# Performance work log

Measured on AMD Instinct MI355X. Metric: run time of the kernel, lower is better.

The kernel has to match this reference:

```python
import jax, jax.numpy as jnp
import numpy as np

B, S, D, H, HD = 8, 1024, 1152, 16, 72
L, R = 32, 36  # get_decompose_dim(1152)
W_BITS, A_BITS = 4, 8


def _ste_round(x):
    return x + jax.lax.stop_gradient(jnp.round(x) - x)


def _fake_quant(x, bits):
    # symmetric fake quant, per last-dim group (per-token for acts, per-out-channel for weights)
    qmax = 2.0 ** (bits - 1) - 1.0
    scale = jnp.maximum(jnp.max(jnp.abs(x), axis=-1, keepdims=True) / qmax, 1e-8)
    return jnp.clip(_ste_round(x / scale), -qmax - 1.0, qmax) * scale


def _kron_apply(x, A, Bm):
    # DecomposeTransMatrix: x (..., L*R) -> reshape (L,R), Y = A^T X B (row-vector kron transform)
    sh = x.shape
    y = jnp.einsum('...lr,lp,rq->...pq', x.reshape(sh[:-1] + (L, R)), A, Bm)
    return y.reshape(sh)


def setup_inputs() -> dict:
    key = jax.random.key(0)
    ks = jax.random.split(key, 16)
    lin = lambda k, sh: jax.random.normal(k, sh, jnp.float32) * 0.02
    return {
        'hidden_states': jax.random.normal(ks[0], (B, S, D), jnp.float32),
        'Wq': lin(ks[1], (D, D)), 'bq': lin(ks[2], (D,)),
        'Wk': lin(ks[3], (D, D)), 'bk': lin(ks[4], (D,)),
        'Wv': lin(ks[5], (D, D)), 'bv': lin(ks[6], (D,)),
        'Wo': lin(ks[7], (D, D)), 'bo': lin(ks[8], (D,)),
        'ln_A': jnp.eye(L, dtype=jnp.float32) + 0.02 * jax.random.normal(ks[9], (L, L), jnp.float32),
        'ln_B': jnp.eye(R, dtype=jnp.float32) + 0.02 * jax.random.normal(ks[10], (R, R), jnp.float32),
        'ln_diag': 1.0 + 0.1 * jax.random.uniform(ks[11], (D,), jnp.float32),
        'vc': jnp.eye(HD, dtype=jnp.float32) + 0.02 * jax.random.normal(ks[12], (HD, HD), jnp.float32),
        'o_mat': jnp.eye(H, dtype=jnp.float32) + 0.02 * jax.random.normal(ks[13], (H, H), jnp.float32),
    }


def reference(hidden_states, Wq, bq, Wk, bk, Wv, bv, Wo, bo, ln_A, ln_B, ln_diag, vc, o_mat):
    invA_T = jnp.linalg.inv(ln_A).T
    invB_T = jnp.linalg.inv(ln_B).T
    # ln_trans applied to activations (diag scale + decomposed Kronecker rotation)
    x = _kron_apply(hidden_states * ln_diag, ln_A, ln_B)  # (B,S,D)

    def qlinear(xin, W, b, out_vc=None):
        # qa_trans inv_t folded into weight: W' = kron(W/diag, invA.T, invB.T) over input dim
        Wt = _kron_apply(W * (1.0 / ln_diag), invA_T, invB_T)
        bt = b
        if out_vc is not None:  # vc_trans folded into to_v output channels
            Wt = jnp.einsum('hdi,de->hei', Wt.reshape(H, HD, D), out_vc).reshape(D, D)
            bt = (b.reshape(H, HD) @ out_vc).reshape(-1)
        return _fake_quant(xin, A_BITS) @ _fake_quant(Wt, W_BITS).T + bt

    q = qlinear(x, Wq, bq).reshape(B, S, H, HD).transpose(0, 2, 1, 3)  # (B,H,S,HD)
    k = qlinear(x, Wk, bk).reshape(B, S, H, HD).transpose(0, 2, 1, 3)
    v = qlinear(x, Wv, bv, out_vc=vc).reshape(B, S, H, HD).transpose(0, 2, 1, 3)

    # baddbmm with beta=0, alpha=1: NO 1/sqrt(d) scaling (faithful to source)
    scores = jnp.einsum('bhqd,bhkd->bhqk', q, k)
    attn = jax.nn.softmax(scores.astype(jnp.float32), axis=-1).astype(q.dtype)
    ctx = jnp.einsum('bhqk,bhkd->bhqd', attn, v).transpose(0, 2, 1, 3)  # (B,S,H,HD)

    # o_trans: matmul(o_mat.T, Y) per token
    ctx = jnp.einsum('bsgd,gh->bshd', ctx, o_mat).reshape(B, S, D)

    # to_out with qa_trans=[inv(O).T, inv(V).T] folded into weight
    o_it = jnp.linalg.inv(o_mat).T
    v_it = jnp.linalg.inv(vc).T
    Wot = jnp.einsum('gh,ogd,de->ohe', o_it, Wo.reshape(D, H, HD), v_it).reshape(D, D)
    out = _fake_quant(ctx, A_BITS) @ _fake_quant(Wot, W_BITS).T + bo
    return out  # rescale_output_factor = 1.0
```

## Files before the change

kernel.cpp:

```cpp
#include <hip/hip_runtime.h>
#include <hip/hip_bf16.h>

#define BB 8
#define SS 1024
#define DD 1152
#define HH 16
#define HD 72
#define PD 96
#define LL 32
#define RR 36
#define NTOK (BB*SS)

typedef __attribute__((ext_vector_type(8)))  short short8;
typedef __attribute__((ext_vector_type(4)))  float f32x4;
typedef __attribute__((ext_vector_type(16))) float f32x16;
typedef __attribute__((ext_vector_type(4)))  unsigned short ushort4v;

#define F_IAT   0
#define F_IBT   1024
#define F_IO    2320
#define F_IV    2576
#define F_BVT   7760
#define F_SX    16384
#define F_SWQ   24576
#define F_SWK   25728
#define F_SWV   26880
#define F_SWO   28032
#define F_SCTX  32768
#define B_R1    1048576ULL
#define B_WB    (B_R1 + 37748736ULL)
#define B_XB    (B_WB + 4ULL*2654208ULL)
#define B_QB    (B_XB + 18874368ULL)
#define B_KB    (B_QB + 25165824ULL)
#define B_VB    (B_KB + 25165824ULL)
#define B_VT    (B_VB + 25165824ULL)
#define WSLOT   1327104ULL

__device__ __forceinline__ unsigned bf16rne(float f) {
    unsigned u = __builtin_bit_cast(unsigned, f);
    return (u + 0x7fffu + ((u >> 16) & 1u)) >> 16;
}
__device__ __forceinline__ unsigned cvtpk(float lo, float hi) {
    unsigned r;
    asm("v_cvt_pk_bf16_f32 %0, %1, %2" : "=v"(r) : "v"(lo), "v"(hi));
    return r;
}
__device__ __forceinline__ short8 mk8(unsigned a, unsigned b, unsigned c, unsigned d) {
    union { unsigned u[4]; short8 s; } t;
    t.u[0] = a; t.u[1] = b; t.u[2] = c; t.u[3] = d;
    return t.s;
}
__device__ __forceinline__ void async_ld16(void* lds, const void* g) {
    __builtin_amdgcn_global_load_lds((const __attribute__((address_space(1))) unsigned*)g,
                                     (__attribute__((address_space(3))) unsigned*)lds, 16, 0, 0);
}

__global__ __launch_bounds__(128) void invert_kernel(const float* __restrict__ A32, const float* __restrict__ B36,
                                                     const float* __restrict__ O16, const float* __restrict__ V72,
                                                     float* __restrict__ ws)
{
    __shared__ float As[80*76], Xs[80*76], Ys[80*76], Ps[80*76], Wt[80*76];
    int which = blockIdx.x;
    int n; const float* src;
    if (which == 0)      { n = 32; src = A32; }
    else if (which == 1) { n = 36; src = B36; }
    else if (which == 2) { n = 16; src = O16; }
    else                 { n = 72; src = V72; }
    int tid = threadIdx.x;
    int nq = n >> 2;
    for (int idx = tid; idx < n*n; idx += 128) {
        int i = idx / n, j = idx % n;
        float a = src[idx];
        As[i*76 + j] = a;
        Xs[i*76 + j] = (i == j ? 2.0f : 0.0f) - a;
    }
    __syncthreads();
    int ty = tid >> 3, qq = tid & 7;

#define NSGEMM(DST, SA, SB) { \
    f32x4 c00={0,0,0,0},c01={0,0,0,0},c02={0,0,0,0}, \
          c10={0,0,0,0},c11={0,0,0,0},c12={0,0,0,0}, \
          c20={0,0,0,0},c21={0,0,0,0},c22={0,0,0,0}, \
          c30={0,0,0,0},c31={0,0,0,0},c32={0,0,0,0}, \
          c40={0,0,0,0},c41={0,0,0,0},c42={0,0,0,0}; \
    _Pragma("unroll 2") \
    for (int k = 0; k < n; ++k) { \
        const float* sb = &SB[k*76]; \
        f32x4 b0 = *(const f32x4*)(sb + 4*qq); \
        f32x4 b1 = *(const f32x4*)(sb + 4*qq + 32); \
        f32x4 b2 = *(const f32x4*)(sb + 4*qq + 64); \
        float a0 = SA[ty*76 + k]; \
        float a1 = SA[(ty+16)*76 + k]; \
        float a2 = SA[(ty+32)*76 + k]; \
        float a3 = SA[(ty+48)*76 + k]; \
        float a4 = SA[(ty+64)*76 + k]; \
        c00 += a0*b0; c01 += a0*b1; c02 += a0*b2; \
        c10 += a1*b0; c11 += a1*b1; c12 += a1*b2; \
        c20 += a2*b0; c21 += a2*b1; c22 += a2*b2; \
        c30 += a3*b0; c31 += a3*b1; c32 += a3*b2; \
        c40 += a4*b0; c41 += a4*b1; c42 += a4*b2; \
    } \
    { \
        f32x4 cc[5][3] = {{c00,c01,c02},{c10,c11,c12},{c20,c21,c22},{c30,c31,c32},{c40,c41,c42}}; \
        _Pragma("unroll") \
        for (int m = 0; m < 5; ++m) { \
            int i = ty + 16*m; \
            if (i < n) { \
                _Pragma("unroll") \
                for (int c = 0; c < 3; ++c) { \
                    int q = qq + 8*c; \
                    if (q < nq) *(f32x4*)&DST[i*76 + 4*q] = cc[m][c]; \
                } \
            } \
        } \
    } \
}
#define NSELEM(P_, Y_) { \
    for (int idx = tid; idx < n*n; idx += 128) { \
        int i = idx / n, j = idx % n; \
        P_[i*76 + j] = P_[i*76 + j] - 3.0f*Y_[i*76 + j] + (i == j ? 3.0f : 0.0f); \
    } \
}
    float* Xc = Xs;
    float* Xn = Wt;
    for (int it = 0; it < 3; ++it) {
        NSGEMM(Ys, As, Xc); __syncthreads();
        NSGEMM(Ps, Ys, Ys); __syncthreads();
        NSELEM(Ps, Ys);     __syncthreads();
        NSGEMM(Xn, Xc, Ps); __syncthreads();
        float* t = Xc; Xc = Xn; Xn = t;
    }
#undef NSGEMM
#undef NSELEM
    if (which == 0) {
        for (int idx = tid; idx < 32*32; idx += 128) { int l = idx/32, pp = idx%32; ws[F_IAT + idx] = Xc[pp*76 + l]; }
    } else if (which == 1) {
        for (int idx = tid; idx < 36*36; idx += 128) { int r = idx/36, qx = idx%36; ws[F_IBT + idx] = Xc[qx*76 + r]; }
    } else if (which == 2) {
        for (int idx = tid; idx < 16*16; idx += 128) { int i = idx/16, j = idx%16; ws[F_IO + idx] = Xc[i*76 + j]; }
    } else {
        for (int idx = tid; idx < 72*72; idx += 128) { int i = idx/72, j = idx%72; ws[F_IV + idx] = Xc[i*76 + j]; }
    }
}

__global__ __launch_bounds__(256) void kron_act_q(const float* __restrict__ src, unsigned short* __restrict__ dst,
                                                  float* __restrict__ scl,
                                                  const float* __restrict__ P, const float* __restrict__ Q,
                                                  const float* __restrict__ diag)
{
    __shared__ float Xs[LL*RR], T1[LL*RR], Ps[LL*LL], Qs[RR*RR], Ys[LL*RR], red[256];
    int row = blockIdx.x;
    int tid = threadIdx.x;
    const float* sr = src + (size_t)row*DD;
    for (int i = tid; i < LL*LL; i += 256) Ps[i] = P[i];
    for (int i = tid; i < RR*RR; i += 256) Qs[i] = Q[i];
    for (int i = tid; i < DD; i += 256) Xs[i] = sr[i]*diag[i];
    __syncthreads();
    for (int s = tid; s < 288; s += 256) {
        int p = s / 9, r4 = (s % 9)*4;
        f32x4 acc = {0.f,0.f,0.f,0.f};
        #pragma unroll 8
        for (int l = 0; l < LL; ++l) {
            float a = Ps[l*LL + p];
            f32x4 x = *(const f32x4*)&Xs[l*RR + r4];
            acc += a*x;
        }
        *(f32x4*)&T1[p*RR + r4] = acc;
    }
    __syncthreads();
    float lmax = 0.f;
    for (int s = tid; s < 288; s += 256) {
        int p = s / 9, q4 = (s % 9)*4;
        f32x4 acc = {0.f,0.f,0.f,0.f};
        #pragma unroll 9
        for (int r = 0; r < RR; ++r) {
            float t = T1[p*RR + r];
            f32x4 qv = *(const f32x4*)&Qs[r*RR + q4];
            acc += t*qv;
        }
        *(f32x4*)&Ys[p*RR + q4] = acc;
        lmax = fmaxf(lmax, fmaxf(fmaxf(fabsf(acc[0]), fabsf(acc[1])), fmaxf(fabsf(acc[2]), fabsf(acc[3]))));
    }
    red[tid] = lmax; __syncthreads();
    for (int s = 128; s > 0; s >>= 1) { if (tid < s) red[tid] = fmaxf(red[tid], red[tid+s]); __syncthreads(); }
    float scale = fmaxf(red[0]/127.f, 1e-8f);
    float rs = 1.f/scale;
    if (tid == 0) scl[row] = scale;
    for (int s = tid; s < 288; s += 256) {
        int i4 = s*4;
        f32x4 y = *(const f32x4*)&Ys[i4];
        ushort4v o;
        #pragma unroll
        for (int c = 0; c < 4; ++c) {
            float v = rintf(y[c]*rs);
            v = fminf(fmaxf(v, -128.f), 127.f);
            o[c] = (unsigned short)bf16rne(v);
        }
        *(ushort4v*)&dst[(size_t)row*DD + i4] = o;
    }
}

__global__ __launch_bounds__(256) void kron_w3(const float* __restrict__ Wq, const float* __restrict__ Wk,
                                               const float* __restrict__ Wv,
                                               unsigned short* __restrict__ Wq_b, unsigned short* __restrict__ Wk_b,
                                               float* __restrict__ Wvm,
                                               float* __restrict__ s_wq, float* __restrict__ s_wk,
                                               const float* __restrict__ P, const float* __restrict__ Q,
                                               const float* __restrict__ diag)
{
    __shared__ float Xs[LL*RR], T1[LL*RR], Ps[LL*LL], Qs[RR*RR], Ys[LL*RR], red[256];
    int z = blockIdx.x / DD;
    int row = blockIdx.x % DD;
    const float* src = (z == 0) ? Wq : (z == 1) ? Wk : Wv;
    int tid = threadIdx.x;
    const float* sr = src + (size_t)row*DD;
    for (int i = tid; i < LL*LL; i += 256) Ps[i] = P[i];
    for (int i = tid; i < RR*RR; i += 256) Qs[i] = Q[i];
    for (int i = tid; i < DD; i += 256) Xs[i] = sr[i]*(1.0f/diag[i]);
    __syncthreads();
    for (int s = tid; s < 288; s += 256) {
        int p = s / 9, r4 = (s % 9)*4;
        f32x4 acc = {0.f,0.f,0.f,0.f};
        #pragma unroll 8
        for (int l = 0; l < LL; ++l) {
            float a = Ps[l*LL + p];
            f32x4 x = *(const f32x4*)&Xs[l*RR + r4];
            acc += a*x;
        }
        *(f32x4*)&T1[p*RR + r4] = acc;
    }
    __syncthreads();
    float lmax = 0.f;
    for (int s = tid; s < 288; s += 256) {
        int p = s / 9, q4 = (s % 9)*4;
        f32x4 acc = {0.f,0.f,0.f,0.f};
        #pragma unroll 9
        for (int r = 0; r < RR; ++r) {
            float t = T1[p*RR + r];
            f32x4 qv = *(const f32x4*)&Qs[r*RR + q4];
            acc += t*qv;
        }
        *(f32x4*)&Ys[p*RR + q4] = acc;
        lmax = fmaxf(lmax, fmaxf(fmaxf(fabsf(acc[0]), fabsf(acc[1])), fmaxf(fabsf(acc[2]), fabsf(acc[3]))));
    }
    if (z == 2) {
        __syncthreads();
        for (int s = tid; s < 288; s += 256) {
            int i4 = s*4;
            *(f32x4*)&Wvm[(size_t)row*DD + i4] = *(const f32x4*)&Ys[i4];
        }
        return;
    }
    red[tid] = lmax; __syncthreads();
    for (int s = 128; s > 0; s >>= 1) { if (tid < s) red[tid] = fmaxf(red[tid], red[tid+s]); __syncthreads(); }
    float scale = fmaxf(red[0]/7.f, 1e-8f);
    float rs = 1.f/scale;
    float* scl = (z == 0) ? s_wq : s_wk;
    unsigned short* dst = (z == 0) ? Wq_b : Wk_b;
    if (tid == 0) scl[row] = scale;
    for (int s = tid; s < 288; s += 256) {
        int i4 = s*4;
        f32x4 y = *(const f32x4*)&Ys[i4];
        ushort4v o;
        #pragma unroll
        for (int c = 0; c < 4; ++c) {
            float v = rintf(y[c]*rs);
            v = fminf(fmaxf(v, -8.f), 7.f);
            o[c] = (unsigned short)bf16rne(v);
        }
        *(ushort4v*)&dst[(size_t)row*DD + i4] = o;
    }
}

__global__ __launch_bounds__(256) void wv_fold_q(const float* __restrict__ tmp, const float* __restrict__ vc,
                                                 const float* __restrict__ bv, unsigned short* __restrict__ dst,
                                                 float* __restrict__ scl, float* __restrict__ bvt)
{
    int he = blockIdx.x;
    int h = he / HD, e = he % HD;
    __shared__ float vcol[HD], Ys[DD], red[256];
    int tid = threadIdx.x;
    if (tid < HD) vcol[tid] = vc[tid*HD + e];
    __syncthreads();
    const float* base = tmp + (size_t)h*HD*DD;
    float lmax = 0.f;
    for (int i = tid; i < DD; i += 256) {
        float acc = 0.f;
        #pragma unroll 8
        for (int d = 0; d < HD; ++d) acc += base[(size_t)d*DD + i]*vcol[d];
        Ys[i] = acc;
        lmax = fmaxf(lmax, fabsf(acc));
    }
    red[tid] = lmax; __syncthreads();
    for (int s = 128; s > 0; s >>= 1) { if (tid < s) red[tid] = fmaxf(red[tid], red[tid+s]); __syncthreads(); }
    float scale = fmaxf(red[0]/7.f, 1e-8f);
    float rs = 1.f/scale;
    if (tid == 0) {
        scl[he] = scale;
        float acc = 0.f;
        for (int d = 0; d < HD; ++d) acc += bv[h*HD + d]*vcol[d];
        bvt[he] = acc;
    }
    for (int i = tid; i < DD; i += 256) {
        float v = rintf(Ys[i]*rs);
        v = fminf(fmaxf(v, -8.f), 7.f);
        dst[(size_t)he*DD + i] = (unsigned short)bf16rne(v);
    }
}

__global__ __launch_bounds__(256) void wo_trans_q(const float* __restrict__ Wo, const float* __restrict__ iO,
                                                  const float* __restrict__ iV, unsigned short* __restrict__ dst,
                                                  float* __restrict__ scl)
{
    __shared__ float M[HH*HD], T1[HH*HD], iOs[HH*HH], iVs[HD*HD], Ys[DD], red[256];
    int row = blockIdx.x, tid = threadIdx.x;
    for (int i = tid; i < DD; i += 256) M[i] = Wo[(size_t)row*DD + i];
    for (int i = tid; i < HH*HH; i += 256) iOs[i] = iO[i];
    for (int i = tid; i < HD*HD; i += 256) iVs[i] = iV[i];
    __syncthreads();
    for (int i = tid; i < DD; i += 256) {
        int h = i / HD, d = i % HD;
        float a = 0.f;
        #pragma unroll
        for (int g = 0; g < HH; ++g) a += iOs[h*HH + g]*M[g*HD + d];
        T1[i] = a;
    }
    __syncthreads();
    float lmax = 0.f;
    for (int i = tid; i < DD; i += 256) {
        int h = i / HD, e = i % HD;
        float a = 0.f;
        #pragma unroll 8
        for (int d = 0; d < HD; ++d) a += T1[h*HD + d]*iVs[e*HD + d];
        Ys[i] = a;
        lmax = fmaxf(lmax, fabsf(a));
    }
    red[tid] = lmax; __syncthreads();
    for (int s = 128; s > 0; s >>= 1) { if (tid < s) red[tid] = fmaxf(red[tid], red[tid+s]); __syncthreads(); }
    float scale = fmaxf(red[0]/7.f, 1e-8f);
    float rs = 1.f/scale;
    if (tid == 0) scl[row] = scale;
    for (int i = tid; i < DD; i += 256) {
        float v = rintf(Ys[i]*rs);
        v = fminf(fmaxf(v, -8.f), 7.f);
        dst[(size_t)row*DD + i] = (unsigned short)bf16rne(v);
    }
}

#define GEMM_STAGE(As, Bs, bufo, k0_, Xb, Wb, tid) { \
    _Pragma("unroll") for (int j_ = 0; j_ < 2; ++j_) { \
        int idx_ = (tid) + j_*256; \
        int row_ = idx_ >> 2, pp_ = idx_ & 3; \
        int s_ = pp_ ^ ((row_ >> 1) & 3); \
        async_ld16(&As[(bufo) + idx_*8], (Xb) + (size_t)row_*DD + (k0_) + s_*8); \
        async_ld16(&Bs[(bufo) + idx_*8], (Wb) + (size_t)row_*DD + (k0_) + s_*8); \
    } }

__device__ __forceinline__ void gemm_body_db(const unsigned short* __restrict__ Xb, const unsigned short* __restrict__ Wb,
                                             unsigned short* As, unsigned short* Bs, f32x4 (&acc)[4][4],
                                             int wr, int wc, int lr, int lg)
{
    int tid = threadIdx.x;
    GEMM_STAGE(As, Bs, 0, 0, Xb, Wb, tid);
    int cur = 0;
    for (int t = 0; t < 36; ++t) {
        if (t < 35) {
            GEMM_STAGE(As, Bs, (cur^1)*4096, (t+1)*32, Xb, Wb, tid);
            asm volatile("s_waitcnt vmcnt(4)" ::: "memory");
        } else {
            asm volatile("s_waitcnt vmcnt(0)" ::: "memory");
        }
        __builtin_amdgcn_sched_barrier(0);
        __builtin_amdgcn_s_barrier();
        const unsigned short* Ab = &As[cur*4096];
        const unsigned short* Bb = &Bs[cur*4096];
        short8 a[4], bfr[4];
        #pragma unroll
        for (int fr = 0; fr < 4; ++fr) {
            int row = wr*64 + fr*16 + lr;
            a[fr] = *(const short8*)(&Ab[row*32 + (lg ^ ((row>>1)&3))*8]);
        }
        #pragma unroll
        for (int fc = 0; fc < 4; ++fc) {
            int row = wc*64 + fc*16 + lr;
            bfr[fc] = *(const short8*)(&Bb[row*32 + (lg ^ ((row>>1)&3))*8]);
        }
        #pragma unroll
        for (int fr = 0; fr < 4; ++fr)
            #pragma unroll
            for (int fc = 0; fc < 4; ++fc)
                acc[fr][fc] = __builtin_amdgcn_mfma_f32_16x16x32_bf16(a[fr], bfr[fc], acc[fr][fc], 0, 0, 0);
        __builtin_amdgcn_s_barrier();
        cur ^= 1;
    }
}

__global__ __launch_bounds__(256) void gemm_qkv(const unsigned short* __restrict__ X,
                                                const unsigned short* __restrict__ Wq_b,
                                                const unsigned short* __restrict__ Wk_b,
                                                const unsigned short* __restrict__ Wv_b,
                                                const float* __restrict__ sx, const float* __restrict__ ws_all,
                                                const float* __restrict__ bq, const float* __restrict__ bk,
                                                const float* __restrict__ bvt,
                                                unsigned short* __restrict__ qb, unsigned short* __restrict__ kb,
                                                unsigned short* __restrict__ vT)
{
    __shared__ __align__(16) unsigned short smem[16384];
    unsigned short* As = smem;
    unsigned short* Bs = smem + 8192;
    int lin = blockIdx.x;
    int nl = (lin & 7)*216 + (lin >> 3);
    int z = nl / 576;
    int rem = nl - z*576;
    int bm = rem / 9, bn = rem - bm*9;
    const unsigned short* W = (z == 0) ? Wq_b : (z == 1) ? Wk_b : Wv_b;
    const float* sw_ = ws_all + (size_t)z*1152;
    const float* bias = (z == 0) ? bq : (z == 1) ? bk : bvt;
    int tid = threadIdx.x;
    int wave = tid >> 6, lane = tid & 63;
    int wr = wave >> 1, wc = wave & 1;
    int lr = lane & 15, lg = lane >> 4;
    f32x4 acc[4][4];
    #pragma unroll
    for (int i = 0; i < 4; ++i)
        #pragma unroll
        for (int j = 0; j < 4; ++j)
            #pragma unroll
            for (int e = 0; e < 4; ++e) acc[i][j][e] = 0.f;
    gemm_body_db(X + (size_t)bm*128*DD, W + (size_t)bn*128*DD, As, Bs, acc, wr, wc, lr, lg);
    float swn[4], bnv[4];
    #pragma unroll
    for (int fc = 0; fc < 4; ++fc) {
        int n = bn*128 + wc*64 + fc*16 + lr;
        swn[fc] = sw_[n]; bnv[fc] = bias[n];
    }
    if (z <= 1) {
        unsigned short* outQ = (z == 0) ? qb : kb;
        #pragma unroll
        for (int c = 0; c < 2; ++c) {
            __syncthreads();
            if (wr == c) {
                #pragma unroll
                for (int fr = 0; fr < 4; ++fr) {
                    #pragma unroll
                    for (int j = 0; j < 4; ++j) {
                        int rloc = fr*16 + lg*4 + j;
                        float sxm = sx[bm*128 + c*64 + rloc];
                        #pragma unroll
                        for (int fc = 0; fc < 4; ++fc) {
                            int cloc = wc*64 + fc*16 + lr;
                            float v = acc[fr][fc][j]*sxm*swn[fc] + bnv[fc];
                            smem[rloc*128 + cloc] = (unsigned short)bf16rne(v);
                        }
                    }
                }
            }
            __syncthreads();
            #pragma unroll
            for (int it = 0; it < 4; ++it) {
                int idx = tid + it*256;
                int row = idx >> 4, seg = idx & 15;
                size_t g = ((size_t)(bm*128 + c*64 + row))*DD + bn*128 + seg*8;
                *(short8*)(&outQ[g]) = *(const short8*)(&smem[row*128 + seg*8]);
            }
        }
    } else {
        int b = bm >> 3;
        int srow = (bm & 7)*128;
        #pragma unroll
        for (int c = 0; c < 2; ++c) {
            __syncthreads();
            if (wr == c) {
                #pragma unroll
                for (int fr = 0; fr < 4; ++fr) {
                    #pragma unroll
                    for (int j = 0; j < 4; ++j) {
                        int rloc = fr*16 + lg*4 + j;
                        float sxm = sx[bm*128 + c*64 + rloc];
                        #pragma unroll
                        for (int fc = 0; fc < 4; ++fc) {
                            int cloc = wc*64 + fc*16 + lr;
                            float v = acc[fr][fc][j]*sxm*swn[fc] + bnv[fc];
                            smem[rloc*130 + cloc] = (unsigned short)bf16rne(v);
                        }
                    }
                }
            }
            __syncthreads();
            #pragma unroll
            for (int it = 0; it < 4; ++it) {
                int idx = tid + it*256;
                int tok8 = idx & 7, cloc = idx >> 3;
                int n = bn*128 + cloc;
                int h = n / 72, hd = n - h*72;
                unsigned short tmp[8];
                #pragma unroll
                for (int kk = 0; kk < 8; ++kk) tmp[kk] = smem[(tok8*8 + kk)*130 + cloc];
                size_t g = ((size_t)((b*HH + h)*PD + hd))*SS + srow + c*64 + tok8*8;
                *(short8*)(&vT[g]) = *(const short8*)tmp;
            }
        }
    }
}

__global__ __launch_bounds__(256) void gemm_out(const unsigned short* __restrict__ X, const unsigned short* __restrict__ W,
                                                const float* __restrict__ sx, const float* __restrict__ sw_,
                                                const float* __restrict__ bias, float* __restrict__ outF)
{
    __shared__ __align__(16) unsigned short smem[16384];
    unsigned short* As = smem;
    unsigned short* Bs = smem + 8192;
    int lin = blockIdx.x;
    int nl = (lin & 7)*72 + (lin >> 3);
    int bm = nl / 9, bn = nl - bm*9;
    int tid = threadIdx.x;
    int wave = tid >> 6, lane = tid & 63;
    int wr = wave >> 1, wc = wave & 1;
    int lr = lane & 15, lg = lane >> 4;
    f32x4 acc[4][4];
    #pragma unroll
    for (int i = 0; i < 4; ++i)
        #pragma unroll
        for (int j = 0; j < 4; ++j)
            #pragma unroll
            for (int e = 0; e < 4; ++e) acc[i][j][e] = 0.f;
    gemm_body_db(X + (size_t)bm*128*DD, W + (size_t)bn*128*DD, As, Bs, acc, wr, wc, lr, lg);
    #pragma unroll
    for (int fc = 0; fc < 4; ++fc) {
        int n = bn*128 + wc*64 + fc*16 + lr;
        float swn = sw_[n], bnv = bias[n];
        #pragma unroll
        for (int fr = 0; fr < 4; ++fr) {
            #pragma unroll
            for (int j = 0; j < 4; ++j) {
                int mrow = bm*128 + wr*64 + fr*16 + lg*4 + j;
                outF[(size_t)mrow*DD + n] = acc[fr][fc][j]*sx[mrow]*swn + bnv;
            }
        }
    }
}

__global__ __launch_bounds__(256) void attn_mfma(const unsigned short* __restrict__ q, const unsigned short* __restrict__ k,
                                                 const unsigned short* __restrict__ vT, float* __restrict__ ctx)
{
    __shared__ unsigned short Kl[64*128];
    __shared__ unsigned short Vl[96*64];
    int lin = blockIdx.x;
    int nl = (lin & 7)*128 + (lin >> 3);
    int bh = nl >> 3;
    int qblk = nl & 7;
    int tid = threadIdx.x;
    int wave = tid >> 6, lane = tid & 63;
    int lq = lane & 31, half = lane >> 5;
    int b = bh >> 4, h = bh & 15;
    const unsigned short* qrow = q + ((size_t)(b*SS + qblk*128 + wave*32 + lq))*DD + h*HD;
    const unsigned short* kbb  = k + (size_t)b*SS*DD + h*HD;
    const unsigned short* vtb  = vT + (size_t)bh*PD*SS;
    short8 zero8 = {0,0,0,0,0,0,0,0};
    short8 qf[6];
    #pragma unroll
    for (int ks = 0; ks < 4; ++ks)
        qf[ks] = *(const short8*)(qrow + ks*16 + half*8);
    qf[4] = (half == 0) ? *(const short8*)(qrow + 64) : zero8;
    qf[5] = zero8;
    for (int idx = tid; idx < 192; idx += 256) {
        int row = idx / 3, s = 9 + idx % 3;
        *(short8*)(&Kl[row*128 + (s ^ (row & 7))*8]) = zero8;
    }
    for (int idx = tid; idx < 192; idx += 256) {
        int d = 72 + (idx >> 3), p = idx & 7;
        *(short8*)(&Vl[d*64 + p*8]) = zero8;
    }
    f32x16 O0, O1, O2;
    #pragma unroll
    for (int r = 0; r < 16; ++r) { O0[r] = 0.f; O1[r] = 0.f; O2[r] = 0.f; }
    float m = -1e30f, l = 0.f;
    for (int t0 = 0; t0 < SS; t0 += 64) {
        __syncthreads();
        for (int idx = tid; idx < 576; idx += 256) {
            int row = idx / 9, s = idx % 9;
            short8 val = *(const short8*)(kbb + (size_t)(t0 + row)*DD + s*8);
            *(short8*)(&Kl[row*128 + (s ^ (row & 7))*8]) = val;
        }
        for (int idx = tid; idx < 576; idx += 256) {
            int d = idx >> 3, p = idx & 7;
            int s = p ^ (d & 7);
            short8 val = *(const short8*)(vtb + (size_t)d*SS + t0 + s*8);
            *(short8*)(&Vl[d*64 + p*8]) = val;
        }
        __syncthreads();
        #pragma unroll
        for (int sub = 0; sub < 2; ++sub) {
            f32x16 sacc;
            #pragma unroll
            for (int r = 0; r < 16; ++r) sacc[r] = 0.f;
            __builtin_amdgcn_s_setprio(1);
            #pragma unroll
            for (int ks = 0; ks < 6; ++ks) {
                int key = sub*32 + lq;
                short8 kf = *(const short8*)(&Kl[key*128 + (((ks*2 + half) ^ (lq & 7)))*8]);
                sacc = __builtin_amdgcn_mfma_f32_32x32x16_bf16(kf, qf[ks], sacc, 0, 0, 0);
            }
            __builtin_amdgcn_s_setprio(0);
            float pa = fmaxf(fmaxf(sacc[0], sacc[1]), fmaxf(sacc[2], sacc[3]));
            float pb = fmaxf(fmaxf(sacc[4], sacc[5]), fmaxf(sacc[6], sacc[7]));
            float pc = fmaxf(fmaxf(sacc[8], sacc[9]), fmaxf(sacc[10], sacc[11]));
            float pd = fmaxf(fmaxf(sacc[12], sacc[13]), fmaxf(sacc[14], sacc[15]));
            float pmax = fmaxf(fmaxf(pa, pb), fmaxf(pc, pd));
            pmax = fmaxf(pmax, __shfl_xor(pmax, 32));
            if (!__all(pmax - m <= 8.0f)) {
                float mn = fmaxf(m, pmax);
                float corr = __expf(m - mn);
                m = mn;
                l *= corr;
                #pragma unroll
                for (int r = 0; r < 16; ++r) {
                    int rowq = (r&3) + 8*(r>>2) + 4*half;
                    float cr = __shfl(corr, rowq);
                    O0[r] *= cr; O1[r] *= cr; O2[r] *= cr;
                }
            }
            float p[16]; float ls = 0.f;
            #pragma unroll
            for (int r = 0; r < 16; ++r) { p[r] = __expf(sacc[r] - m); ls += p[r]; }
            ls += __shfl_xor(ls, 32);
            l += ls;
            unsigned pk[8], sw[8];
            #pragma unroll
            for (int j2 = 0; j2 < 8; ++j2) pk[j2] = cvtpk(p[2*j2], p[2*j2+1]);
            #pragma unroll
            for (int j2 = 0; j2 < 8; ++j2) sw[j2] = __shfl_xor(pk[j2], 32);
            short8 A0 = half ? mk8(sw[2], sw[3], pk[2], pk[3]) : mk8(pk[0], pk[1], sw[0], sw[1]);
            short8 A1 = half ? mk8(sw[6], sw[7], pk[6], pk[7]) : mk8(pk[4], pk[5], sw[4], sw[5]);
            __builtin_amdgcn_s_setprio(1);
            #pragma unroll
            for (int dt = 0; dt < 3; ++dt) {
                int d = dt*32 + lq;
                short8 vf0 = *(const short8*)(&Vl[d*64 + (((sub*4 + half) ^ (d & 7)))*8]);
                short8 vf1 = *(const short8*)(&Vl[d*64 + (((sub*4 + 2 + half) ^ (d & 7)))*8]);
                if (dt == 0) { O0 = __builtin_amdgcn_mfma_f32_32x32x16_bf16(A0, vf0, O0, 0,0,0);
                               O0 = __builtin_amdgcn_mfma_f32_32x32x16_bf16(A1, vf1, O0, 0,0,0); }
                if (dt == 1) { O1 = __builtin_amdgcn_mfma_f32_32x32x16_bf16(A0, vf0, O1, 0,0,0);
                               O1 = __builtin_amdgcn_mfma_f32_32x32x16_bf16(A1, vf1, O1, 0,0,0); }
                if (dt == 2) { O2 = __builtin_amdgcn_mfma_f32_32x32x16_bf16(A0, vf0, O2, 0,0,0);
                               O2 = __builtin_amdgcn_mfma_f32_32x32x16_bf16(A1, vf1, O2, 0,0,0); }
            }
            __builtin_amdgcn_s_setprio(0);
        }
    }
    float linv = 1.f / l;
    #pragma unroll
    for (int r = 0; r < 16; ++r) {
        int rowq = (r&3) + 8*(r>>2) + 4*half;
        float lr2 = __shfl(linv, rowq);
        int s = qblk*128 + wave*32 + rowq;
        size_t base = ((size_t)(b*SS + s))*DD + h*HD;
        ctx[base + lq]      = O0[r]*lr2;
        ctx[base + 32 + lq] = O1[r]*lr2;
        if (lq < 8) ctx[base + 64 + lq] = O2[r]*lr2;
    }
}

__global__ __launch_bounds__(256) void octx_fq_q(const float* __restrict__ ctx, const float* __restrict__ o_mat,
                                                 unsigned short* __restrict__ out, float* __restrict__ scl)
{
    __shared__ float ct[DD], Ys[DD], om[HH*HH], red[256];
    int t = blockIdx.x, tid = threadIdx.x;
    for (int i = tid; i < DD; i += 256) ct[i] = ctx[(size_t)t*DD + i];
    for (int i = tid; i < HH*HH; i += 256) om[i] = o_mat[i];
    __syncthreads();
    float lmax = 0.f;
    for (int s = tid; s < 288; s += 256) {
        int h = s / 18, d4 = (s % 18)*4;
        f32x4 acc = {0.f,0.f,0.f,0.f};
        #pragma unroll
        for (int g = 0; g < HH; ++g) {
            float o = om[g*HH + h];
            f32x4 c = *(const f32x4*)&ct[g*HD + d4];
            acc += o*c;
        }
        *(f32x4*)&Ys[h*HD + d4] = acc;
        lmax = fmaxf(lmax, fmaxf(fmaxf(fabsf(acc[0]), fabsf(acc[1])), fmaxf(fabsf(acc[2]), fabsf(acc[3]))));
    }
    red[tid] = lmax; __syncthreads();
    for (int s = 128; s > 0; s >>= 1) { if (tid < s) red[tid] = fmaxf(red[tid], red[tid+s]); __syncthreads(); }
    float scale = fmaxf(red[0]/127.f, 1e-8f);
    float rs = 1.f/scale;
    if (tid == 0) scl[t] = scale;
    for (int s = tid; s < 288; s += 256) {
        int i4 = s*4;
        f32x4 y = *(const f32x4*)&Ys[i4];
        ushort4v o;
        #pragma unroll
        for (int c = 0; c < 4; ++c) {
            float v = rintf(y[c]*rs);
            v = fminf(fmaxf(v, -128.f), 127.f);
            o[c] = (unsigned short)bf16rne(v);
        }
        *(ushort4v*)&out[(size_t)t*DD + i4] = o;
    }
}

extern "C" void kernel_launch(void* const* d_in, const int* in_sizes, int n_in,
                              void* d_out, int out_size, void* d_ws, size_t ws_size,
                              hipStream_t stream)
{
    const float* hidden = (const float*)d_in[0];
    const float* Wq = (const float*)d_in[1];  const float* bq = (const float*)d_in[2];
    const float* Wk = (const float*)d_in[3];  const float* bk = (const float*)d_in[4];
    const float* Wv = (const float*)d_in[5];  const float* bv = (const float*)d_in[6];
    const float* Wo = (const float*)d_in[7];  const float* bo = (const float*)d_in[8];
    const float* lnA = (const float*)d_in[9];
    const float* lnB = (const float*)d_in[10];
    const float* ln_diag = (const float*)d_in[11];
    const float* vc = (const float*)d_in[12];
    const float* o_mat = (const float*)d_in[13];
    float* ws = (float*)d_ws;
    float* out = (float*)d_out;
    char* wsb = (char*)d_ws;

    float* iAT  = ws + F_IAT;
    float* iBT  = ws + F_IBT;
    float* iO   = ws + F_IO;
    float* iV   = ws + F_IV;
    float* bvt  = ws + F_BVT;
    float* s_x  = ws + F_SX;
    float* s_wq = ws + F_SWQ;
    float* s_wk = ws + F_SWK;
    float* s_wv = ws + F_SWV;
    float* s_wo = ws + F_SWO;
    float* s_ct = ws + F_SCTX;

    float* slot = (float*)(wsb + B_R1);
    float* Wvm  = slot + 2*WSLOT;
    float* ctxf = slot;

    unsigned short* Wq_b = (unsigned short*)(wsb + B_WB);
    unsigned short* Wk_b = Wq_b + WSLOT;
    unsigned short* Wv_b = Wq_b + 2*WSLOT;
    unsigned short* Wo_b = Wq_b + 3*WSLOT;
    unsigned short* x_b  = (unsigned short*)(wsb + B_XB);
    unsigned short* ctx_b = x_b;
    unsigned short* qb = (unsigned short*)(wsb + B_QB);
    unsigned short* kb = (unsigned short*)(wsb + B_KB);
    unsigned short* vT = (unsigned short*)(wsb + B_VT);

    invert_kernel<<<4, 128, 0, stream>>>(lnA, lnB, o_mat, vc, ws);
    kron_act_q<<<NTOK, 256, 0, stream>>>(hidden, x_b, s_x, lnA, lnB, ln_diag);
    kron_w3<<<3*DD, 256, 0, stream>>>(Wq, Wk, Wv, Wq_b, Wk_b, Wvm, s_wq, s_wk, iAT, iBT, ln_diag);
    wv_fold_q<<<DD, 256, 0, stream>>>(Wvm, vc, bv, Wv_b, s_wv, bvt);
    wo_trans_q<<<DD, 256, 0, stream>>>(Wo, iO, iV, Wo_b, s_wo);
    gemm_qkv<<<dim3(1728), 256, 0, stream>>>(x_b, Wq_b, Wk_b, Wv_b, s_x, s_wq, bq, bk, bvt, qb, kb, vT);
    attn_mfma<<<dim3(1024), 256, 0, stream>>>(qb, kb, vT, ctxf);
    octx_fq_q<<<NTOK, 256, 0, stream>>>(ctxf, o_mat, ctx_b, s_ct);
    gemm_out<<<dim3(576), 256, 0, stream>>>(ctx_b, Wo_b, s_ct, s_wo, bo, out);
}
```

Baseline: 597.1 us.

## Prefetch next K/V tile into registers and process full 64-key tile per softmax step

The attention loop now loads the next K and V tile from global memory into registers while the current tile is being computed, then writes those registers to LDS at the start of the next iteration. The two 32-key subtiles are merged into a single softmax update over 64 keys, halving the max/rescale/sum reductions and the online-softmax correction passes. This adds register pressure from the prefetch buffers and the doubled score and probability arrays, which may reduce occupancy or cause spills.

```diff
diff --git a/kernel.cpp b/kernel.cpp
--- a/kernel.cpp
+++ b/kernel.cpp
@@ -571,83 +571,129 @@
         int d = 72 + (idx >> 3), p = idx & 7;
         *(short8*)(&Vl[d*64 + p*8]) = zero8;
     }
+    short8 kr[3], vr[3];
+#define ATT_LOAD(T0) { \
+    _Pragma("unroll") for (int j_ = 0; j_ < 3; ++j_) { \
+        int idx_ = tid + j_*256; \
+        if (idx_ < 576) { \
+            int row_ = idx_ / 9, s_ = idx_ - row_*9; \
+            kr[j_] = *(const short8*)(kbb + (size_t)((T0) + row_)*DD + s_*8); \
+        } \
+    } \
+    _Pragma("unroll") for (int j_ = 0; j_ < 3; ++j_) { \
+        int idx_ = tid + j_*256; \
+        if (idx_ < 576) { \
+            int d_ = idx_ >> 3, p_ = idx_ & 7, s_ = p_ ^ (d_ & 7); \
+            vr[j_] = *(const short8*)(vtb + (size_t)d_*SS + (T0) + s_*8); \
+        } \
+    } }
+#define ATT_WRITE() { \
+    _Pragma("unroll") for (int j_ = 0; j_ < 3; ++j_) { \
+        int idx_ = tid + j_*256; \
+        if (idx_ < 576) { \
+            int row_ = idx_ / 9, s_ = idx_ - row_*9; \
+            *(short8*)(&Kl[row_*128 + (s_ ^ (row_ & 7))*8]) = kr[j_]; \
+        } \
+    } \
+    _Pragma("unroll") for (int j_ = 0; j_ < 3; ++j_) { \
+        int idx_ = tid + j_*256; \
+        if (idx_ < 576) { \
+            int d_ = idx_ >> 3, p_ = idx_ & 7; \
+            *(short8*)(&Vl[d_*64 + p_*8]) = vr[j_]; \
+        } \
+    } }
     f32x16 O0, O1, O2;
     #pragma unroll
     for (int r = 0; r < 16; ++r) { O0[r] = 0.f; O1[r] = 0.f; O2[r] = 0.f; }
     float m = -1e30f, l = 0.f;
+    ATT_LOAD(0);
     for (int t0 = 0; t0 < SS; t0 += 64) {
         __syncthreads();
-        for (int idx = tid; idx < 576; idx += 256) {
-            int row = idx / 9, s = idx % 9;
-            short8 val = *(const short8*)(kbb + (size_t)(t0 + row)*DD + s*8);
-            *(short8*)(&Kl[row*128 + (s ^ (row & 7))*8]) = val;
-        }
-        for (int idx = tid; idx < 576; idx += 256) {
-            int d = idx >> 3, p = idx & 7;
-            int s = p ^ (d & 7);
-            short8 val = *(const short8*)(vtb + (size_t)d*SS + t0 + s*8);
-            *(short8*)(&Vl[d*64 + p*8]) = val;
-        }
+        ATT_WRITE();
         __syncthreads();
-        #pragma unroll
-        for (int sub = 0; sub < 2; ++sub) {
-            f32x16 sacc;
+        if (t0 + 64 < SS) ATT_LOAD(t0 + 64);
+        f32x16 s0, s1;
+        #pragma unroll
+        for (int r = 0; r < 16; ++r) { s0[r] = 0.f; s1[r] = 0.f; }
+        __builtin_amdgcn_s_setprio(1);
+        #pragma unroll
+        for (int ks = 0; ks < 6; ++ks) {
+            short8 kf = *(const short8*)(&Kl[lq*128 + (((ks*2 + half) ^ (lq & 7)))*8]);
+            s0 = __builtin_amdgcn_mfma_f32_32x32x16_bf16(kf, qf[ks], s0, 0, 0, 0);
+        }
+        #pragma unroll
+        for (int ks = 0; ks < 6; ++ks) {
+            int key = 32 + lq;
+            short8 kf = *(const short8*)(&Kl[key*128 + (((ks*2 + half) ^ (lq & 7)))*8]);
+            s1 = __builtin_amdgcn_mfma_f32_32x32x16_bf16(kf, qf[ks], s1, 0, 0, 0);
+        }
+        __builtin_amdgcn_s_setprio(0);
+        float pa = fmaxf(fmaxf(s0[0], s0[1]), fmaxf(s0[2], s0[3]));
+        float pb = fmaxf(fmaxf(s0[4], s0[5]), fmaxf(s0[6], s0[7]));
+        float pc = fmaxf(fmaxf(s0[8], s0[9]), fmaxf(s0[10], s0[11]));
+        float pd = fmaxf(fmaxf(s0[12], s0[13]), fmaxf(s0[14], s0[15]));
+        float pe = fmaxf(fmaxf(s1[0], s1[1]), fmaxf(s1[2], s1[3]));
+        float pf = fmaxf(fmaxf(s1[4], s1[5]), fmaxf(s1[6], s1[7]));
+        float pg = fmaxf(fmaxf(s1[8], s1[9]), fmaxf(s1[10], s1[11]));
+        float ph = fmaxf(fmaxf(s1[12], s1[13]), fmaxf(s1[14], s1[15]));
+        float pmax = fmaxf(fmaxf(fmaxf(pa, pb), fmaxf(pc, pd)),
+                           fmaxf(fmaxf(pe, pf), fmaxf(pg, ph)));
+        pmax = fmaxf(pmax, __shfl_xor(pmax, 32));
+        if (!__all(pmax - m <= 8.0f)) {
+            float mn = fmaxf(m, pmax);
+            float corr = __expf(m - mn);
+            m = mn;
+            l *= corr;
             #pragma unroll
-            for (int r = 0; r < 16; ++r) sacc[r] = 0.f;
-            __builtin_amdgcn_s_setprio(1);
-            #pragma unroll
-            for (int ks = 0; ks < 6; ++ks) {
-                int key = sub*32 + lq;
-                short8 kf = *(const short8*)(&Kl[key*128 + (((ks*2 + half) ^ (lq & 7)))*8]);
-                sacc = __builtin_amdgcn_mfma_f32_32x32x16_bf16(kf, qf[ks], sacc, 0, 0, 0);
+            for (int r = 0; r < 16; ++r) {
+                int rowq = (r&3) + 8*(r>>2) + 4*half;
+                float cr = __shfl(corr, rowq);
+                O0[r] *= cr; O1[r] *= cr; O2[r] *= cr;
             }
-            __builtin_amdgcn_s_setprio(0);
-            float pa = fmaxf(fmaxf(sacc[0], sacc[1]), fmaxf(sacc[2], sacc[3]));
-            float pb = fmaxf(fmaxf(sacc[4], sacc[5]), fmaxf(sacc[6], sacc[7]));
-            float pc = fmaxf(fmaxf(sacc[8], sacc[9]), fmaxf(sacc[10], sacc[11]));
-            float pd = fmaxf(fmaxf(sacc[12], sacc[13]), fmaxf(sacc[14], sacc[15]));
-            float pmax = fmaxf(fmaxf(pa, pb), fmaxf(pc, pd));
-            pmax = fmaxf(pmax, __shfl_xor(pmax, 32));
-            if (!__all(pmax - m <= 8.0f)) {
-                float mn = fmaxf(m, pmax);
-                float corr = __expf(m - mn);
-                m = mn;
-                l *= corr;
-                #pragma unroll
-                for (int r = 0; r < 16; ++r) {
-                    int rowq = (r&3) + 8*(r>>2) + 4*half;
-                    float cr = __shfl(corr, rowq);
-                    O0[r] *= cr; O1[r] *= cr; O2[r] *= cr;
-                }
-            }
-            float p[16]; float ls = 0.f;
-            #pragma unroll
-            for (int r = 0; r < 16; ++r) { p[r] = __expf(sacc[r] - m); ls += p[r]; }
-            ls += __shfl_xor(ls, 32);
-            l += ls;
-            unsigned pk[8], sw[8];
-            #pragma unroll
-            for (int j2 = 0; j2 < 8; ++j2) pk[j2] = cvtpk(p[2*j2], p[2*j2+1]);
-            #pragma unroll
-            for (int j2 = 0; j2 < 8; ++j2) sw[j2] = __shfl_xor(pk[j2], 32);
-            short8 A0 = half ? mk8(sw[2], sw[3], pk[2], pk[3]) : mk8(pk[0], pk[1], sw[0], sw[1]);
-            short8 A1 = half ? mk8(sw[6], sw[7], pk[6], pk[7]) : mk8(pk[4], pk[5], sw[4], sw[5]);
-            __builtin_amdgcn_s_setprio(1);
-            #pragma unroll
-            for (int dt = 0; dt < 3; ++dt) {
-                int d = dt*32 + lq;
-                short8 vf0 = *(const short8*)(&Vl[d*64 + (((sub*4 + half) ^ (d & 7)))*8]);
-                short8 vf1 = *(const short8*)(&Vl[d*64 + (((sub*4 + 2 + half) ^ (d & 7)))*8]);
-                if (dt == 0) { O0 = __builtin_amdgcn_mfma_f32_32x32x16_bf16(A0, vf0, O0, 0,0,0);
-                               O0 = __builtin_amdgcn_mfma_f32_32x32x16_bf16(A1, vf1, O0, 0,0,0); }
-                if (dt == 1) { O1 = __builtin_amdgcn_mfma_f32_32x32x16_bf16(A0, vf0, O1, 0,0,0);
-                               O1 = __builtin_amdgcn_mfma_f32_32x32x16_bf16(A1, vf1, O1, 0,0,0); }
-                if (dt == 2) { O2 = __builtin_amdgcn_mfma_f32_32x32x16_bf16(A0, vf0, O2, 0,0,0);
-                               O2 = __builtin_amdgcn_mfma_f32_32x32x16_bf16(A1, vf1, O2, 0,0,0); }
-            }
-            __builtin_amdgcn_s_setprio(0);
-        }
-    }
+        }
+        float p0[16], p1[16];
+        float ls = 0.f, ls1 = 0.f;
+        #pragma unroll
+        for (int r = 0; r < 16; ++r) { p0[r] = __expf(s0[r] - m); p1[r] = __expf(s1[r] - m); }
+        #pragma unroll
+        for (int r = 0; r < 16; ++r) { ls += p0[r]; ls1 += p1[r]; }
+        ls += ls1;
+        ls += __shfl_xor(ls, 32);
+        l += ls;
+        unsigned pk0[8], sw0[8], pk1[8], sw1[8];
+        #pragma unroll
+        for (int j2 = 0; j2 < 8; ++j2) { pk0[j2] = cvtpk(p0[2*j2], p0[2*j2+1]); pk1[j2] = cvtpk(p1[2*j2], p1[2*j2+1]); }
+        #pragma unroll
+        for (int j2 = 0; j2 < 8; ++j2) { sw0[j2] = __shfl_xor(pk0[j2], 32); sw1[j2] = __shfl_xor(pk1[j2], 32); }
+        short8 A0 = half ? mk8(sw0[2], sw0[3], pk0[2], pk0[3]) : mk8(pk0[0], pk0[1], sw0[0], sw0[1]);
+        short8 A1 = half ? mk8(sw0[6], sw0[7], pk0[6], pk0[7]) : mk8(pk0[4], pk0[5], sw0[4], sw0[5]);
+        short8 A2 = half ? mk8(sw1[2], sw1[3], pk1[2], pk1[3]) : mk8(pk1[0], pk1[1], sw1[0], sw1[1]);
+        short8 A3 = half ? mk8(sw1[6], sw1[7], pk1[6], pk1[7]) : mk8(pk1[4], pk1[5], sw1[4], sw1[5]);
+        __builtin_amdgcn_s_setprio(1);
+        #pragma unroll
+        for (int dt = 0; dt < 3; ++dt) {
+            int d = dt*32 + lq;
+            short8 vf0 = *(const short8*)(&Vl[d*64 + (((half)     ^ (d & 7)))*8]);
+            short8 vf1 = *(const short8*)(&Vl[d*64 + (((2 + half) ^ (d & 7)))*8]);
+            short8 vf2 = *(const short8*)(&Vl[d*64 + (((4 + half) ^ (d & 7)))*8]);
+            short8 vf3 = *(const short8*)(&Vl[d*64 + (((6 + half) ^ (d & 7)))*8]);
+            if (dt == 0) { O0 = __builtin_amdgcn_mfma_f32_32x32x16_bf16(A0, vf0, O0, 0,0,0);
+                           O0 = __builtin_amdgcn_mfma_f32_32x32x16_bf16(A1, vf1, O0, 0,0,0);
+                           O0 = __builtin_amdgcn_mfma_f32_32x32x16_bf16(A2, vf2, O0, 0,0,0);
+                           O0 = __builtin_amdgcn_mfma_f32_32x32x16_bf16(A3, vf3, O0, 0,0,0); }
+            if (dt == 1) { O1 = __builtin_amdgcn_mfma_f32_32x32x16_bf16(A0, vf0, O1, 0,0,0);
+                           O1 = __builtin_amdgcn_mfma_f32_32x32x16_bf16(A1, vf1, O1, 0,0,0);
+                           O1 = __builtin_amdgcn_mfma_f32_32x32x16_bf16(A2, vf2, O1, 0,0,0);
+                           O1 = __builtin_amdgcn_mfma_f32_32x32x16_bf16(A3, vf3, O1, 0,0,0); }
+            if (dt == 2) { O2 = __builtin_amdgcn_mfma_f32_32x32x16_bf16(A0, vf0, O2, 0,0,0);
+                           O2 = __builtin_amdgcn_mfma_f32_32x32x16_bf16(A1, vf1, O2, 0,0,0);
+                           O2 = __builtin_amdgcn_mfma_f32_32x32x16_bf16(A2, vf2, O2, 0,0,0);
+                           O2 = __builtin_amdgcn_mfma_f32_32x32x16_bf16(A3, vf3, O2, 0,0,0); }
+        }
+        __builtin_amdgcn_s_setprio(0);
+    }
+#undef ATT_LOAD
+#undef ATT_WRITE
     float linv = 1.f / l;
     #pragma unroll
     for (int r = 0; r < 16; ++r) {
```

New measurement: 610.9 us. 2.3% more time.
